# Kernel tuning notes

Hardware: AMD Instinct MI355X
Metric: run time of the kernel (lower is better)

The kernel has to match this reference:

```python
import jax, jax.numpy as jnp
import numpy as np

CODEBOOK_SIZE = 1024
EMBED_DIM = 64
COMMITMENT_COST = 0.25


def setup_inputs() -> dict:
    key = jax.random.key(0)
    k1, k2 = jax.random.split(key)
    z = jax.random.normal(k1, (8, EMBED_DIM, 8192), dtype=jnp.float32)
    # torch init: uniform(-1/codebook_size, 1/codebook_size)
    codebook_weight = jax.random.uniform(
        k2, (CODEBOOK_SIZE, EMBED_DIM), dtype=jnp.float32,
        minval=-1.0 / CODEBOOK_SIZE, maxval=1.0 / CODEBOOK_SIZE)
    return {"z": z, "codebook_weight": codebook_weight}


def reference(z, codebook_weight):
    B, D, T = z.shape
    # [B*T, D]
    z_flat = jnp.transpose(z, (0, 2, 1)).reshape(-1, D)
    # squared euclidean distances to each code: ||z||^2 - 2 z.W^T + ||W||^2
    distances = (jnp.sum(z_flat * z_flat, axis=1, keepdims=True)
                 - 2.0 * z_flat @ codebook_weight.T
                 + jnp.sum(codebook_weight * codebook_weight, axis=1))
    codes = jnp.argmin(distances, axis=1)  # [B*T]
    z_q = codebook_weight[codes].reshape(B, T, D).transpose(0, 2, 1)  # [B, D, T]
    commitment_loss = jnp.mean((jax.lax.stop_gradient(z_q) - z) ** 2)
    codebook_loss = jnp.mean((z_q - jax.lax.stop_gradient(z)) ** 2)
    vq_loss = codebook_loss + COMMITMENT_COST * commitment_loss
    # straight-through estimator
    z_q_st = z + jax.lax.stop_gradient(z_q - z)
    return z_q_st, vq_loss, codes
```

## Files before the change

### kernel.cpp

```cpp
#include <hip/hip_runtime.h>


#define T_DIM 8192
#define D_DIM 64
#define C_DIM 1024
#define B_DIM 8
#define NROWS (B_DIM * T_DIM)
#define NELEM (B_DIM * D_DIM * T_DIM)
#define NBLKS (NROWS / 256)

#define R64(M) M(0) M(1) M(2) M(3) M(4) M(5) M(6) M(7) \
  M(8) M(9) M(10) M(11) M(12) M(13) M(14) M(15) \
  M(16) M(17) M(18) M(19) M(20) M(21) M(22) M(23) \
  M(24) M(25) M(26) M(27) M(28) M(29) M(30) M(31) \
  M(32) M(33) M(34) M(35) M(36) M(37) M(38) M(39) \
  M(40) M(41) M(42) M(43) M(44) M(45) M(46) M(47) \
  M(48) M(49) M(50) M(51) M(52) M(53) M(54) M(55) \
  M(56) M(57) M(58) M(59) M(60) M(61) M(62) M(63)

#define SQ_(x) __fmul_rn(x, x)
#define AD_(a, b) __fadd_rn(a, b)

#define PAIRWISE64(p, dst) \
  float pr0 = SQ_(p##0);  pr0 = AD_(pr0, SQ_(p##8));  pr0 = AD_(pr0, SQ_(p##16)); pr0 = AD_(pr0, SQ_(p##24)); pr0 = AD_(pr0, SQ_(p##32)); pr0 = AD_(pr0, SQ_(p##40)); pr0 = AD_(pr0, SQ_(p##48)); pr0 = AD_(pr0, SQ_(p##56)); \
  float pr1 = SQ_(p##1);  pr1 = AD_(pr1, SQ_(p##9));  pr1 = AD_(pr1, SQ_(p##17)); pr1 = AD_(pr1, SQ_(p##25)); pr1 = AD_(pr1, SQ_(p##33)); pr1 = AD_(pr1, SQ_(p##41)); pr1 = AD_(pr1, SQ_(p##49)); pr1 = AD_(pr1, SQ_(p##57)); \
  float pr2 = SQ_(p##2);  pr2 = AD_(pr2, SQ_(p##10)); pr2 = AD_(pr2, SQ_(p##18)); pr2 = AD_(pr2, SQ_(p##26)); pr2 = AD_(pr2, SQ_(p##34)); pr2 = AD_(pr2, SQ_(p##42)); pr2 = AD_(pr2, SQ_(p##50)); pr2 = AD_(pr2, SQ_(p##58)); \
  float pr3 = SQ_(p##3);  pr3 = AD_(pr3, SQ_(p##11)); pr3 = AD_(pr3, SQ_(p##19)); pr3 = AD_(pr3, SQ_(p##27)); pr3 = AD_(pr3, SQ_(p##35)); pr3 = AD_(pr3, SQ_(p##43)); pr3 = AD_(pr3, SQ_(p##51)); pr3 = AD_(pr3, SQ_(p##59)); \
  float pr4 = SQ_(p##4);  pr4 = AD_(pr4, SQ_(p##12)); pr4 = AD_(pr4, SQ_(p##20)); pr4 = AD_(pr4, SQ_(p##28)); pr4 = AD_(pr4, SQ_(p##36)); pr4 = AD_(pr4, SQ_(p##44)); pr4 = AD_(pr4, SQ_(p##52)); pr4 = AD_(pr4, SQ_(p##60)); \
  float pr5 = SQ_(p##5);  pr5 = AD_(pr5, SQ_(p##13)); pr5 = AD_(pr5, SQ_(p##21)); pr5 = AD_(pr5, SQ_(p##29)); pr5 = AD_(pr5, SQ_(p##37)); pr5 = AD_(pr5, SQ_(p##45)); pr5 = AD_(pr5, SQ_(p##53)); pr5 = AD_(pr5, SQ_(p##61)); \
  float pr6 = SQ_(p##6);  pr6 = AD_(pr6, SQ_(p##14)); pr6 = AD_(pr6, SQ_(p##22)); pr6 = AD_(pr6, SQ_(p##30)); pr6 = AD_(pr6, SQ_(p##38)); pr6 = AD_(pr6, SQ_(p##46)); pr6 = AD_(pr6, SQ_(p##54)); pr6 = AD_(pr6, SQ_(p##62)); \
  float pr7 = SQ_(p##7);  pr7 = AD_(pr7, SQ_(p##15)); pr7 = AD_(pr7, SQ_(p##23)); pr7 = AD_(pr7, SQ_(p##31)); pr7 = AD_(pr7, SQ_(p##39)); pr7 = AD_(pr7, SQ_(p##47)); pr7 = AD_(pr7, SQ_(p##55)); pr7 = AD_(pr7, SQ_(p##63)); \
  float dst = AD_(AD_(AD_(pr0, pr1), AD_(pr2, pr3)), AD_(AD_(pr4, pr5), AD_(pr6, pr7)));

#define WSQ_OF(arr, dst) float dst; { \
  float c0 = SQ_(arr[0].x); c0=AD_(c0,SQ_(arr[2].x)); c0=AD_(c0,SQ_(arr[4].x)); c0=AD_(c0,SQ_(arr[6].x)); c0=AD_(c0,SQ_(arr[8].x)); c0=AD_(c0,SQ_(arr[10].x)); c0=AD_(c0,SQ_(arr[12].x)); c0=AD_(c0,SQ_(arr[14].x)); \
  float c1 = SQ_(arr[0].y); c1=AD_(c1,SQ_(arr[2].y)); c1=AD_(c1,SQ_(arr[4].y)); c1=AD_(c1,SQ_(arr[6].y)); c1=AD_(c1,SQ_(arr[8].y)); c1=AD_(c1,SQ_(arr[10].y)); c1=AD_(c1,SQ_(arr[12].y)); c1=AD_(c1,SQ_(arr[14].y)); \
  float c2 = SQ_(arr[0].z); c2=AD_(c2,SQ_(arr[2].z)); c2=AD_(c2,SQ_(arr[4].z)); c2=AD_(c2,SQ_(arr[6].z)); c2=AD_(c2,SQ_(arr[8].z)); c2=AD_(c2,SQ_(arr[10].z)); c2=AD_(c2,SQ_(arr[12].z)); c2=AD_(c2,SQ_(arr[14].z)); \
  float c3 = SQ_(arr[0].w); c3=AD_(c3,SQ_(arr[2].w)); c3=AD_(c3,SQ_(arr[4].w)); c3=AD_(c3,SQ_(arr[6].w)); c3=AD_(c3,SQ_(arr[8].w)); c3=AD_(c3,SQ_(arr[10].w)); c3=AD_(c3,SQ_(arr[12].w)); c3=AD_(c3,SQ_(arr[14].w)); \
  float c4 = SQ_(arr[1].x); c4=AD_(c4,SQ_(arr[3].x)); c4=AD_(c4,SQ_(arr[5].x)); c4=AD_(c4,SQ_(arr[7].x)); c4=AD_(c4,SQ_(arr[9].x)); c4=AD_(c4,SQ_(arr[11].x)); c4=AD_(c4,SQ_(arr[13].x)); c4=AD_(c4,SQ_(arr[15].x)); \
  float c5 = SQ_(arr[1].y); c5=AD_(c5,SQ_(arr[3].y)); c5=AD_(c5,SQ_(arr[5].y)); c5=AD_(c5,SQ_(arr[7].y)); c5=AD_(c5,SQ_(arr[9].y)); c5=AD_(c5,SQ_(arr[11].y)); c5=AD_(c5,SQ_(arr[13].y)); c5=AD_(c5,SQ_(arr[15].y)); \
  float c6 = SQ_(arr[1].z); c6=AD_(c6,SQ_(arr[3].z)); c6=AD_(c6,SQ_(arr[5].z)); c6=AD_(c6,SQ_(arr[7].z)); c6=AD_(c6,SQ_(arr[9].z)); c6=AD_(c6,SQ_(arr[11].z)); c6=AD_(c6,SQ_(arr[13].z)); c6=AD_(c6,SQ_(arr[15].z)); \
  float c7 = SQ_(arr[1].w); c7=AD_(c7,SQ_(arr[3].w)); c7=AD_(c7,SQ_(arr[5].w)); c7=AD_(c7,SQ_(arr[7].w)); c7=AD_(c7,SQ_(arr[9].w)); c7=AD_(c7,SQ_(arr[11].w)); c7=AD_(c7,SQ_(arr[13].w)); c7=AD_(c7,SQ_(arr[15].w)); \
  dst = AD_(AD_(AD_(c0, c1), AD_(c2, c3)), AD_(AD_(c4, c5), AD_(c6, c7))); }

__global__ __launch_bounds__(512, 2)
void vq_fused_kernel(const float* __restrict__ z,
                     const float* __restrict__ cb,
                     float* __restrict__ out,
                     float* __restrict__ codes,
                     double* __restrict__ partials) {
    const int tid  = threadIdx.x;
    const int wid  = tid >> 6;
    const int lane = tid & 63;
    const int row0 = blockIdx.x * 256;
    const int b    = row0 >> 13;
    const int t0   = row0 & (T_DIM - 1);

    __shared__ float4 zl[16][256];
    __shared__ float  zsql[256];
    __shared__ float2 res[8][256];
    __shared__ int    codesl[256];

    if (tid < 256) {
        const float* zp = z + (size_t)b * (D_DIM * T_DIM) + (t0 + tid);
#define LOADZ(k) float z##k = zp[(size_t)k * T_DIM];
        R64(LOADZ)
#undef LOADZ
        PAIRWISE64(z, zsq)
        zsql[tid] = zsq;
        zl[ 0][tid] = make_float4(z0,  z1,  z2,  z3);
        zl[ 1][tid] = make_float4(z4,  z5,  z6,  z7);
        zl[ 2][tid] = make_float4(z8,  z9,  z10, z11);
        zl[ 3][tid] = make_float4(z12, z13, z14, z15);
        zl[ 4][tid] = make_float4(z16, z17, z18, z19);
        zl[ 5][tid] = make_float4(z20, z21, z22, z23);
        zl[ 6][tid] = make_float4(z24, z25, z26, z27);
        zl[ 7][tid] = make_float4(z28, z29, z30, z31);
        zl[ 8][tid] = make_float4(z32, z33, z34, z35);
        zl[ 9][tid] = make_float4(z36, z37, z38, z39);
        zl[10][tid] = make_float4(z40, z41, z42, z43);
        zl[11][tid] = make_float4(z44, z45, z46, z47);
        zl[12][tid] = make_float4(z48, z49, z50, z51);
        zl[13][tid] = make_float4(z52, z53, z54, z55);
        zl[14][tid] = make_float4(z56, z57, z58, z59);
        zl[15][tid] = make_float4(z60, z61, z62, z63);
    }

    const int cbase = wid * 128;
    const int cA = cbase + lane;
    const int cB = cA + 64;
    float4 wa[16], wb[16];
    {
        const float4* wpa = (const float4*)(cb + ((size_t)cA << 6));
        const float4* wpb = (const float4*)(cb + ((size_t)cB << 6));
#pragma unroll
        for (int kk = 0; kk < 16; ++kk) { wa[kk] = wpa[kk]; wb[kk] = wpb[kk]; }
    }
    WSQ_OF(wa, wsqA)
    WSQ_OF(wb, wsqB)
    __syncthreads();

#pragma unroll 1
    for (int r = 0; r < 256; r += 4) {
        float aA0 = 0.f, aA1 = 0.f, aA2 = 0.f, aA3 = 0.f;
        float aB0 = 0.f, aB1 = 0.f, aB2 = 0.f, aB3 = 0.f;
#pragma unroll
        for (int kk = 0; kk < 16; ++kk) {
            const float4 zc0 = zl[kk][r + 0];
            const float4 zc1 = zl[kk][r + 1];
            const float4 zc2 = zl[kk][r + 2];
            const float4 zc3 = zl[kk][r + 3];
            const float4 WA = wa[kk];
            const float4 WB = wb[kk];
            aA0 = fmaf(zc0.x, WA.x, aA0); aA0 = fmaf(zc0.y, WA.y, aA0);
            aA0 = fmaf(zc0.z, WA.z, aA0); aA0 = fmaf(zc0.w, WA.w, aA0);
            aB0 = fmaf(zc0.x, WB.x, aB0); aB0 = fmaf(zc0.y, WB.y, aB0);
            aB0 = fmaf(zc0.z, WB.z, aB0); aB0 = fmaf(zc0.w, WB.w, aB0);
            aA1 = fmaf(zc1.x, WA.x, aA1); aA1 = fmaf(zc1.y, WA.y, aA1);
            aA1 = fmaf(zc1.z, WA.z, aA1); aA1 = fmaf(zc1.w, WA.w, aA1);
            aB1 = fmaf(zc1.x, WB.x, aB1); aB1 = fmaf(zc1.y, WB.y, aB1);
            aB1 = fmaf(zc1.z, WB.z, aB1); aB1 = fmaf(zc1.w, WB.w, aB1);
            aA2 = fmaf(zc2.x, WA.x, aA2); aA2 = fmaf(zc2.y, WA.y, aA2);
            aA2 = fmaf(zc2.z, WA.z, aA2); aA2 = fmaf(zc2.w, WA.w, aA2);
            aB2 = fmaf(zc2.x, WB.x, aB2); aB2 = fmaf(zc2.y, WB.y, aB2);
            aB2 = fmaf(zc2.z, WB.z, aB2); aB2 = fmaf(zc2.w, WB.w, aB2);
            aA3 = fmaf(zc3.x, WA.x, aA3); aA3 = fmaf(zc3.y, WA.y, aA3);
            aA3 = fmaf(zc3.z, WA.z, aA3); aA3 = fmaf(zc3.w, WA.w, aA3);
            aB3 = fmaf(zc3.x, WB.x, aB3); aB3 = fmaf(zc3.y, WB.y, aB3);
            aB3 = fmaf(zc3.z, WB.z, aB3); aB3 = fmaf(zc3.w, WB.w, aB3);
        }
        const float zr0 = zsql[r + 0];
        const float zr1 = zsql[r + 1];
        const float zr2 = zsql[r + 2];
        const float zr3 = zsql[r + 3];
        const float dA0 = __fadd_rn(__fsub_rn(zr0, __fmul_rn(2.0f, aA0)), wsqA);
        const float dB0 = __fadd_rn(__fsub_rn(zr0, __fmul_rn(2.0f, aB0)), wsqB);
        const float dA1 = __fadd_rn(__fsub_rn(zr1, __fmul_rn(2.0f, aA1)), wsqA);
        const float dB1 = __fadd_rn(__fsub_rn(zr1, __fmul_rn(2.0f, aB1)), wsqB);
        const float dA2 = __fadd_rn(__fsub_rn(zr2, __fmul_rn(2.0f, aA2)), wsqA);
        const float dB2 = __fadd_rn(__fsub_rn(zr2, __fmul_rn(2.0f, aB2)), wsqB);
        const float dA3 = __fadd_rn(__fsub_rn(zr3, __fmul_rn(2.0f, aA3)), wsqA);
        const float dB3 = __fadd_rn(__fsub_rn(zr3, __fmul_rn(2.0f, aB3)), wsqB);
        const bool tB0 = (dB0 < dA0); const float d0 = tB0 ? dB0 : dA0;
        const bool tB1 = (dB1 < dA1); const float d1 = tB1 ? dB1 : dA1;
        const bool tB2 = (dB2 < dA2); const float d2 = tB2 ? dB2 : dA2;
        const bool tB3 = (dB3 < dA3); const float d3 = tB3 ? dB3 : dA3;
        float m0 = d0, m1 = d1, m2 = d2, m3 = d3;
#pragma unroll
        for (int off = 32; off > 0; off >>= 1) {
            m0 = fminf(m0, __shfl_xor(m0, off, 64));
            m1 = fminf(m1, __shfl_xor(m1, off, 64));
            m2 = fminf(m2, __shfl_xor(m2, off, 64));
            m3 = fminf(m3, __shfl_xor(m3, off, 64));
        }
#define ARGMIN_J(mj, dj, tBj, outIdx) { \
        const unsigned long long mskA = __ballot((!tBj) && (dj == mj)); \
        const unsigned long long mskB = __ballot(tBj && (dj == mj)); \
        int code; \
        if (mskA) code = cbase + (__ffsll((long long)mskA) - 1); \
        else      code = cbase + 64 + (__ffsll((long long)mskB) - 1); \
        if (lane == 0) res[wid][outIdx] = make_float2(mj, (float)code); }
        ARGMIN_J(m0, d0, tB0, r + 0)
        ARGMIN_J(m1, d1, tB1, r + 1)
        ARGMIN_J(m2, d2, tB2, r + 2)
        ARGMIN_J(m3, d3, tB3, r + 3)
#undef ARGMIN_J
    }
    __syncthreads();

    if (tid < 256) {
        float2 best = res[0][tid];
#pragma unroll
        for (int w = 1; w < 8; ++w) {
            const float2 p = res[w][tid];
            if (p.x < best.x) best = p;
        }
        codes[row0 + tid] = best.y;
        codesl[tid] = (int)best.y;
    }
    __syncthreads();

    const int hi = tid >> 8;
    const int tl = tid & 255;
    double lsum = 0.0;
    float* outb = out + (size_t)b * (D_DIM * T_DIM);
#pragma unroll 1
    for (int it = 0; it < 32; ++it) {
        const int d = (it << 1) + hi;
        const int code = codesl[tl];
        const float4 zq4 = zl[d >> 2][tl];
        const float zv = (d & 3) == 0 ? zq4.x : (d & 3) == 1 ? zq4.y
                       : (d & 3) == 2 ? zq4.z : zq4.w;
        const float wv = cb[(code << 6) + d];
        const float df = __fsub_rn(wv, zv);
        outb[(size_t)d * T_DIM + (t0 + tl)] = __fadd_rn(zv, df);
        lsum += (double)df * (double)df;
    }
#pragma unroll
    for (int o2 = 32; o2 > 0; o2 >>= 1) lsum += __shfl_down(lsum, o2, 64);
    __shared__ double redd[8];
    if (lane == 0) redd[wid] = lsum;
    __syncthreads();
    if (tid == 0) {
        double t4 = ((redd[0] + redd[1]) + (redd[2] + redd[3]))
                  + ((redd[4] + redd[5]) + (redd[6] + redd[7]));
        partials[blockIdx.x] = t4;
    }
}

__global__ void vq_loss_kernel(const double* __restrict__ partials,
                               float* __restrict__ out_loss) {
    double s = 0.0;
    for (int i = threadIdx.x; i < NBLKS; i += 256) s += partials[i];
#pragma unroll
    for (int o = 32; o > 0; o >>= 1) s += __shfl_down(s, o, 64);
    __shared__ double red[4];
    if ((threadIdx.x & 63) == 0) red[threadIdx.x >> 6] = s;
    __syncthreads();
    if (threadIdx.x == 0) {
        double tot = (red[0] + red[1]) + (red[2] + red[3]);
        out_loss[0] = (float)(1.25 * tot / (double)NELEM);
    }
}

extern "C" void kernel_launch(void* const* d_in, const int* in_sizes, int n_in,
                              void* d_out, int out_size, void* d_ws, size_t ws_size,
                              hipStream_t stream) {
    const float* z  = (const float*)d_in[0];
    const float* cb = (const float*)d_in[1];

    float* out      = (float*)d_out;
    float* out_loss = out + NELEM;
    float* codes    = out + NELEM + 1;

    double* partials = (double*)d_ws;

    vq_fused_kernel<<<NBLKS, 512, 0, stream>>>(z, cb, out, codes, partials);
    vq_loss_kernel<<<1, 256, 0, stream>>>(partials, out_loss);
}
```

Before: 223.8 us.

## Halve block size and give each thread four codebook entries in registers

Each block now runs 256 threads instead of 512, and each wave covers 256 codes (four per lane, held in registers) instead of 128. This doubles the reuse of each shared-memory z read per FMA and halves the cross-wave argmin reduction. The epilogue is also rewritten so each thread handles one row and reads the codebook row as float4. In exchange, register pressure roughly doubles (64 float4 weights plus 16 accumulators) and occupancy drops to one block of 256 threads per launch bound, which risks spills or poor latency hiding.

```diff
diff --git a/kernel.cpp b/kernel.cpp
--- a/kernel.cpp
+++ b/kernel.cpp
@@ -43,7 +43,11 @@
   float c7 = SQ_(arr[1].w); c7=AD_(c7,SQ_(arr[3].w)); c7=AD_(c7,SQ_(arr[5].w)); c7=AD_(c7,SQ_(arr[7].w)); c7=AD_(c7,SQ_(arr[9].w)); c7=AD_(c7,SQ_(arr[11].w)); c7=AD_(c7,SQ_(arr[13].w)); c7=AD_(c7,SQ_(arr[15].w)); \
   dst = AD_(AD_(AD_(c0, c1), AD_(c2, c3)), AD_(AD_(c4, c5), AD_(c6, c7))); }
 
-__global__ __launch_bounds__(512, 2)
+#define FM4(acc, zc, W) \
+    acc = fmaf(zc.x, W.x, acc); acc = fmaf(zc.y, W.y, acc); \
+    acc = fmaf(zc.z, W.z, acc); acc = fmaf(zc.w, W.w, acc);
+
+__global__ __launch_bounds__(256, 1)
 void vq_fused_kernel(const float* __restrict__ z,
                      const float* __restrict__ cb,
                      float* __restrict__ out,
@@ -58,10 +62,10 @@
 
     __shared__ float4 zl[16][256];
     __shared__ float  zsql[256];
-    __shared__ float2 res[8][256];
+    __shared__ float2 res[4][256];
     __shared__ int    codesl[256];
 
-    if (tid < 256) {
+    {
         const float* zp = z + (size_t)b * (D_DIM * T_DIM) + (t0 + tid);
 #define LOADZ(k) float z##k = zp[(size_t)k * T_DIM];
         R64(LOADZ)
@@ -86,24 +90,31 @@
         zl[15][tid] = make_float4(z60, z61, z62, z63);
     }
 
-    const int cbase = wid * 128;
-    const int cA = cbase + lane;
-    const int cB = cA + 64;
-    float4 wa[16], wb[16];
+    const int cbase = wid * 256;
+    float4 wa[16], wb[16], wc[16], wd[16];
     {
-        const float4* wpa = (const float4*)(cb + ((size_t)cA << 6));
-        const float4* wpb = (const float4*)(cb + ((size_t)cB << 6));
-#pragma unroll
-        for (int kk = 0; kk < 16; ++kk) { wa[kk] = wpa[kk]; wb[kk] = wpb[kk]; }
+        const float4* wpa = (const float4*)(cb + ((size_t)(cbase + lane)       << 6));
+        const float4* wpb = (const float4*)(cb + ((size_t)(cbase + lane + 64)  << 6));
+        const float4* wpc = (const float4*)(cb + ((size_t)(cbase + lane + 128) << 6));
+        const float4* wpd = (const float4*)(cb + ((size_t)(cbase + lane + 192) << 6));
+#pragma unroll
+        for (int kk = 0; kk < 16; ++kk) {
+            wa[kk] = wpa[kk]; wb[kk] = wpb[kk];
+            wc[kk] = wpc[kk]; wd[kk] = wpd[kk];
+        }
     }
     WSQ_OF(wa, wsqA)
     WSQ_OF(wb, wsqB)
+    WSQ_OF(wc, wsqC)
+    WSQ_OF(wd, wsqD)
     __syncthreads();
 
 #pragma unroll 1
     for (int r = 0; r < 256; r += 4) {
         float aA0 = 0.f, aA1 = 0.f, aA2 = 0.f, aA3 = 0.f;
         float aB0 = 0.f, aB1 = 0.f, aB2 = 0.f, aB3 = 0.f;
+        float aC0 = 0.f, aC1 = 0.f, aC2 = 0.f, aC3 = 0.f;
+        float aD0 = 0.f, aD1 = 0.f, aD2 = 0.f, aD3 = 0.f;
 #pragma unroll
         for (int kk = 0; kk < 16; ++kk) {
             const float4 zc0 = zl[kk][r + 0];
@@ -112,22 +123,12 @@
             const float4 zc3 = zl[kk][r + 3];
             const float4 WA = wa[kk];
             const float4 WB = wb[kk];
-            aA0 = fmaf(zc0.x, WA.x, aA0); aA0 = fmaf(zc0.y, WA.y, aA0);
-            aA0 = fmaf(zc0.z, WA.z, aA0); aA0 = fmaf(zc0.w, WA.w, aA0);
-            aB0 = fmaf(zc0.x, WB.x, aB0); aB0 = fmaf(zc0.y, WB.y, aB0);
-            aB0 = fmaf(zc0.z, WB.z, aB0); aB0 = fmaf(zc0.w, WB.w, aB0);
-            aA1 = fmaf(zc1.x, WA.x, aA1); aA1 = fmaf(zc1.y, WA.y, aA1);
-            aA1 = fmaf(zc1.z, WA.z, aA1); aA1 = fmaf(zc1.w, WA.w, aA1);
-            aB1 = fmaf(zc1.x, WB.x, aB1); aB1 = fmaf(zc1.y, WB.y, aB1);
-            aB1 = fmaf(zc1.z, WB.z, aB1); aB1 = fmaf(zc1.w, WB.w, aB1);
-            aA2 = fmaf(zc2.x, WA.x, aA2); aA2 = fmaf(zc2.y, WA.y, aA2);
-            aA2 = fmaf(zc2.z, WA.z, aA2); aA2 = fmaf(zc2.w, WA.w, aA2);
-            aB2 = fmaf(zc2.x, WB.x, aB2); aB2 = fmaf(zc2.y, WB.y, aB2);
-            aB2 = fmaf(zc2.z, WB.z, aB2); aB2 = fmaf(zc2.w, WB.w, aB2);
-            aA3 = fmaf(zc3.x, WA.x, aA3); aA3 = fmaf(zc3.y, WA.y, aA3);
-            aA3 = fmaf(zc3.z, WA.z, aA3); aA3 = fmaf(zc3.w, WA.w, aA3);
-            aB3 = fmaf(zc3.x, WB.x, aB3); aB3 = fmaf(zc3.y, WB.y, aB3);
-            aB3 = fmaf(zc3.z, WB.z, aB3); aB3 = fmaf(zc3.w, WB.w, aB3);
+            const float4 WC = wc[kk];
+            const float4 WD = wd[kk];
+            FM4(aA0, zc0, WA) FM4(aA1, zc1, WA) FM4(aA2, zc2, WA) FM4(aA3, zc3, WA)
+            FM4(aB0, zc0, WB) FM4(aB1, zc1, WB) FM4(aB2, zc2, WB) FM4(aB3, zc3, WB)
+            FM4(aC0, zc0, WC) FM4(aC1, zc1, WC) FM4(aC2, zc2, WC) FM4(aC3, zc3, WC)
+            FM4(aD0, zc0, WD) FM4(aD1, zc1, WD) FM4(aD2, zc2, WD) FM4(aD3, zc3, WD)
         }
         const float zr0 = zsql[r + 0];
         const float zr1 = zsql[r + 1];
@@ -135,17 +136,24 @@
         const float zr3 = zsql[r + 3];
         const float dA0 = __fadd_rn(__fsub_rn(zr0, __fmul_rn(2.0f, aA0)), wsqA);
         const float dB0 = __fadd_rn(__fsub_rn(zr0, __fmul_rn(2.0f, aB0)), wsqB);
+        const float dC0 = __fadd_rn(__fsub_rn(zr0, __fmul_rn(2.0f, aC0)), wsqC);
+        const float dD0 = __fadd_rn(__fsub_rn(zr0, __fmul_rn(2.0f, aD0)), wsqD);
         const float dA1 = __fadd_rn(__fsub_rn(zr1, __fmul_rn(2.0f, aA1)), wsqA);
         const float dB1 = __fadd_rn(__fsub_rn(zr1, __fmul_rn(2.0f, aB1)), wsqB);
+        const float dC1 = __fadd_rn(__fsub_rn(zr1, __fmul_rn(2.0f, aC1)), wsqC);
+        const float dD1 = __fadd_rn(__fsub_rn(zr1, __fmul_rn(2.0f, aD1)), wsqD);
         const float dA2 = __fadd_rn(__fsub_rn(zr2, __fmul_rn(2.0f, aA2)), wsqA);
         const float dB2 = __fadd_rn(__fsub_rn(zr2, __fmul_rn(2.0f, aB2)), wsqB);
+        const float dC2 = __fadd_rn(__fsub_rn(zr2, __fmul_rn(2.0f, aC2)), wsqC);
+        const float dD2 = __fadd_rn(__fsub_rn(zr2, __fmul_rn(2.0f, aD2)), wsqD);
         const float dA3 = __fadd_rn(__fsub_rn(zr3, __fmul_rn(2.0f, aA3)), wsqA);
         const float dB3 = __fadd_rn(__fsub_rn(zr3, __fmul_rn(2.0f, aB3)), wsqB);
-        const bool tB0 = (dB0 < dA0); const float d0 = tB0 ? dB0 : dA0;
-        const bool tB1 = (dB1 < dA1); const float d1 = tB1 ? dB1 : dA1;
-        const bool tB2 = (dB2 < dA2); const float d2 = tB2 ? dB2 : dA2;
-        const bool tB3 = (dB3 < dA3); const float d3 = tB3 ? dB3 : dA3;
-        float m0 = d0, m1 = d1, m2 = d2, m3 = d3;
+        const float dC3 = __fadd_rn(__fsub_rn(zr3, __fmul_rn(2.0f, aC3)), wsqC);
+        const float dD3 = __fadd_rn(__fsub_rn(zr3, __fmul_rn(2.0f, aD3)), wsqD);
+        float m0 = fminf(fminf(dA0, dB0), fminf(dC0, dD0));
+        float m1 = fminf(fminf(dA1, dB1), fminf(dC1, dD1));
+        float m2 = fminf(fminf(dA2, dB2), fminf(dC2, dD2));
+        float m3 = fminf(fminf(dA3, dB3), fminf(dC3, dD3));
 #pragma unroll
         for (int off = 32; off > 0; off >>= 1) {
             m0 = fminf(m0, __shfl_xor(m0, off, 64));
@@ -153,25 +161,29 @@
             m2 = fminf(m2, __shfl_xor(m2, off, 64));
             m3 = fminf(m3, __shfl_xor(m3, off, 64));
         }
-#define ARGMIN_J(mj, dj, tBj, outIdx) { \
-        const unsigned long long mskA = __ballot((!tBj) && (dj == mj)); \
-        const unsigned long long mskB = __ballot(tBj && (dj == mj)); \
+#define ARG4(mj, dAj, dBj, dCj, dDj, outIdx) { \
+        const unsigned long long kA = __ballot(dAj == mj); \
+        const unsigned long long kB = __ballot(dBj == mj); \
+        const unsigned long long kC = __ballot(dCj == mj); \
+        const unsigned long long kD = __ballot(dDj == mj); \
         int code; \
-        if (mskA) code = cbase + (__ffsll((long long)mskA) - 1); \
-        else      code = cbase + 64 + (__ffsll((long long)mskB) - 1); \
+        if (kA)      code = cbase +       (__ffsll((long long)kA) - 1); \
+        else if (kB) code = cbase + 64  + (__ffsll((long long)kB) - 1); \
+        else if (kC) code = cbase + 128 + (__ffsll((long long)kC) - 1); \
+        else         code = cbase + 192 + (__ffsll((long long)kD) - 1); \
         if (lane == 0) res[wid][outIdx] = make_float2(mj, (float)code); }
-        ARGMIN_J(m0, d0, tB0, r + 0)
-        ARGMIN_J(m1, d1, tB1, r + 1)
-        ARGMIN_J(m2, d2, tB2, r + 2)
-        ARGMIN_J(m3, d3, tB3, r + 3)
-#undef ARGMIN_J
-    }
-    __syncthreads();
-
-    if (tid < 256) {
+        ARG4(m0, dA0, dB0, dC0, dD0, r + 0)
+        ARG4(m1, dA1, dB1, dC1, dD1, r + 1)
+        ARG4(m2, dA2, dB2, dC2, dD2, r + 2)
+        ARG4(m3, dA3, dB3, dC3, dD3, r + 3)
+#undef ARG4
+    }
+    __syncthreads();
+
+    {
         float2 best = res[0][tid];
 #pragma unroll
-        for (int w = 1; w < 8; ++w) {
+        for (int w = 1; w < 4; ++w) {
             const float2 p = res[w][tid];
             if (p.x < best.x) best = p;
         }
@@ -180,32 +192,32 @@
     }
     __syncthreads();
 
-    const int hi = tid >> 8;
-    const int tl = tid & 255;
+    const int tl = tid;
+    const int code = codesl[tl];
     double lsum = 0.0;
-    float* outb = out + (size_t)b * (D_DIM * T_DIM);
+    float* outb = out + (size_t)b * (D_DIM * T_DIM) + t0 + tl;
 #pragma unroll 1
-    for (int it = 0; it < 32; ++it) {
-        const int d = (it << 1) + hi;
-        const int code = codesl[tl];
-        const float4 zq4 = zl[d >> 2][tl];
-        const float zv = (d & 3) == 0 ? zq4.x : (d & 3) == 1 ? zq4.y
-                       : (d & 3) == 2 ? zq4.z : zq4.w;
-        const float wv = cb[(code << 6) + d];
-        const float df = __fsub_rn(wv, zv);
-        outb[(size_t)d * T_DIM + (t0 + tl)] = __fadd_rn(zv, df);
-        lsum += (double)df * (double)df;
+    for (int it = 0; it < 16; ++it) {
+        const float4 z4 = zl[it][tl];
+        const float4 w4 = *(const float4*)(cb + ((size_t)code << 6) + (it << 2));
+        const float df0 = __fsub_rn(w4.x, z4.x);
+        const float df1 = __fsub_rn(w4.y, z4.y);
+        const float df2 = __fsub_rn(w4.z, z4.z);
+        const float df3 = __fsub_rn(w4.w, z4.w);
+        outb[(size_t)((it << 2) + 0) * T_DIM] = __fadd_rn(z4.x, df0);
+        outb[(size_t)((it << 2) + 1) * T_DIM] = __fadd_rn(z4.y, df1);
+        outb[(size_t)((it << 2) + 2) * T_DIM] = __fadd_rn(z4.z, df2);
+        outb[(size_t)((it << 2) + 3) * T_DIM] = __fadd_rn(z4.w, df3);
+        lsum += (double)df0 * df0 + (double)df1 * df1
+              + (double)df2 * df2 + (double)df3 * df3;
     }
 #pragma unroll
     for (int o2 = 32; o2 > 0; o2 >>= 1) lsum += __shfl_down(lsum, o2, 64);
-    __shared__ double redd[8];
+    __shared__ double redd[4];
     if (lane == 0) redd[wid] = lsum;
     __syncthreads();
-    if (tid == 0) {
-        double t4 = ((redd[0] + redd[1]) + (redd[2] + redd[3]))
-                  + ((redd[4] + redd[5]) + (redd[6] + redd[7]));
-        partials[blockIdx.x] = t4;
-    }
+    if (tid == 0)
+        partials[blockIdx.x] = (redd[0] + redd[1]) + (redd[2] + redd[3]);
 }
 
 __global__ void vq_loss_kernel(const double* __restrict__ partials,
@@ -235,6 +247,6 @@
 
     double* partials = (double*)d_ws;
 
-    vq_fused_kernel<<<NBLKS, 512, 0, stream>>>(z, cb, out, codes, partials);
+    vq_fused_kernel<<<NBLKS, 256, 0, stream>>>(z, cb, out, codes, partials);
     vq_loss_kernel<<<1, 256, 0, stream>>>(partials, out_loss);
 }
```

After: 333.3 us. +48.9%, slower.

## Halve rows per block, load z with all threads, vectorize codebook gather

Applied to the files above, without the earlier changes.

Each block now handles 128 rows instead of 256, doubling the grid and halving shared memory per block, and the launch bounds ask for 4 blocks per CU. All 512 threads cooperatively load z into shared memory instead of only 256, and the output/loss epilogue gathers codebook rows as float4 with fixed per-thread slices. The intent is more occupancy and better latency hiding in the load and epilogue phases. In exchange, every block still loads all 128 codebook vectors per wave into registers, so codebook load and norm work per output row doubles, and the 4-block bound may cause register spills.

```diff
diff --git a/kernel.cpp b/kernel.cpp
--- a/kernel.cpp
+++ b/kernel.cpp
@@ -7,16 +7,8 @@
 #define B_DIM 8
 #define NROWS (B_DIM * T_DIM)
 #define NELEM (B_DIM * D_DIM * T_DIM)
-#define NBLKS (NROWS / 256)
-
-#define R64(M) M(0) M(1) M(2) M(3) M(4) M(5) M(6) M(7) \
-  M(8) M(9) M(10) M(11) M(12) M(13) M(14) M(15) \
-  M(16) M(17) M(18) M(19) M(20) M(21) M(22) M(23) \
-  M(24) M(25) M(26) M(27) M(28) M(29) M(30) M(31) \
-  M(32) M(33) M(34) M(35) M(36) M(37) M(38) M(39) \
-  M(40) M(41) M(42) M(43) M(44) M(45) M(46) M(47) \
-  M(48) M(49) M(50) M(51) M(52) M(53) M(54) M(55) \
-  M(56) M(57) M(58) M(59) M(60) M(61) M(62) M(63)
+#define TROWS 128
+#define NBLKS (NROWS / TROWS)
 
 #define SQ_(x) __fmul_rn(x, x)
 #define AD_(a, b) __fadd_rn(a, b)
@@ -43,7 +35,7 @@
   float c7 = SQ_(arr[1].w); c7=AD_(c7,SQ_(arr[3].w)); c7=AD_(c7,SQ_(arr[5].w)); c7=AD_(c7,SQ_(arr[7].w)); c7=AD_(c7,SQ_(arr[9].w)); c7=AD_(c7,SQ_(arr[11].w)); c7=AD_(c7,SQ_(arr[13].w)); c7=AD_(c7,SQ_(arr[15].w)); \
   dst = AD_(AD_(AD_(c0, c1), AD_(c2, c3)), AD_(AD_(c4, c5), AD_(c6, c7))); }
 
-__global__ __launch_bounds__(512, 2)
+__global__ __launch_bounds__(512, 4)
 void vq_fused_kernel(const float* __restrict__ z,
                      const float* __restrict__ cb,
                      float* __restrict__ out,
@@ -52,47 +44,62 @@
     const int tid  = threadIdx.x;
     const int wid  = tid >> 6;
     const int lane = tid & 63;
-    const int row0 = blockIdx.x * 256;
+    const int row0 = blockIdx.x * TROWS;
     const int b    = row0 >> 13;
     const int t0   = row0 & (T_DIM - 1);
 
-    __shared__ float4 zl[16][256];
-    __shared__ float  zsql[256];
-    __shared__ float2 res[8][256];
-    __shared__ int    codesl[256];
-
-    if (tid < 256) {
-        const float* zp = z + (size_t)b * (D_DIM * T_DIM) + (t0 + tid);
-#define LOADZ(k) float z##k = zp[(size_t)k * T_DIM];
-        R64(LOADZ)
-#undef LOADZ
+    __shared__ float4 zl[16][TROWS];
+    __shared__ float  zsql[TROWS];
+    __shared__ float2 res[8][TROWS];
+    __shared__ int    codesl[TROWS];
+
+    {
+        const int q   = tid >> 7;
+        const int row = tid & (TROWS - 1);
+        const float* zp = z + (size_t)b * (D_DIM * T_DIM)
+                        + (size_t)(q * 16) * T_DIM + (t0 + row);
+#pragma unroll
+        for (int j = 0; j < 4; ++j) {
+            float4 v;
+            v.x = zp[(size_t)(j * 4 + 0) * T_DIM];
+            v.y = zp[(size_t)(j * 4 + 1) * T_DIM];
+            v.z = zp[(size_t)(j * 4 + 2) * T_DIM];
+            v.w = zp[(size_t)(j * 4 + 3) * T_DIM];
+            zl[q * 4 + j][row] = v;
+        }
+    }
+    __syncthreads();
+
+    if (tid < TROWS) {
+        const float4 q0 = zl[0][tid],  q1 = zl[1][tid],  q2 = zl[2][tid],  q3 = zl[3][tid];
+        const float4 q4 = zl[4][tid],  q5 = zl[5][tid],  q6 = zl[6][tid],  q7 = zl[7][tid];
+        const float4 q8 = zl[8][tid],  q9 = zl[9][tid],  q10 = zl[10][tid], q11 = zl[11][tid];
+        const float4 q12 = zl[12][tid], q13 = zl[13][tid], q14 = zl[14][tid], q15 = zl[15][tid];
+        const float z0=q0.x,  z1=q0.y,  z2=q0.z,  z3=q0.w;
+        const float z4=q1.x,  z5=q1.y,  z6=q1.z,  z7=q1.w;
+        const float z8=q2.x,  z9=q2.y,  z10=q2.z, z11=q2.w;
+        const float z12=q3.x, z13=q3.y, z14=q3.z, z15=q3.w;
+        const float z16=q4.x, z17=q4.y, z18=q4.z, z19=q4.w;
+        const float z20=q5.x, z21=q5.y, z22=q5.z, z23=q5.w;
+        const float z24=q6.x, z25=q6.y, z26=q6.z, z27=q6.w;
+        const float z28=q7.x, z29=q7.y, z30=q7.z, z31=q7.w;
+        const float z32=q8.x, z33=q8.y, z34=q8.z, z35=q8.w;
+        const float z36=q9.x, z37=q9.y, z38=q9.z, z39=q9.w;
+        const float z40=q10.x, z41=q10.y, z42=q10.z, z43=q10.w;
+        const float z44=q11.x, z45=q11.y, z46=q11.z, z47=q11.w;
+        const float z48=q12.x, z49=q12.y, z50=q12.z, z51=q12.w;
+        const float z52=q13.x, z53=q13.y, z54=q13.z, z55=q13.w;
+        const float z56=q14.x, z57=q14.y, z58=q14.z, z59=q14.w;
+        const float z60=q15.x, z61=q15.y, z62=q15.z, z63=q15.w;
         PAIRWISE64(z, zsq)
         zsql[tid] = zsq;
-        zl[ 0][tid] = make_float4(z0,  z1,  z2,  z3);
-        zl[ 1][tid] = make_float4(z4,  z5,  z6,  z7);
-        zl[ 2][tid] = make_float4(z8,  z9,  z10, z11);
-        zl[ 3][tid] = make_float4(z12, z13, z14, z15);
-        zl[ 4][tid] = make_float4(z16, z17, z18, z19);
-        zl[ 5][tid] = make_float4(z20, z21, z22, z23);
-        zl[ 6][tid] = make_float4(z24, z25, z26, z27);
-        zl[ 7][tid] = make_float4(z28, z29, z30, z31);
-        zl[ 8][tid] = make_float4(z32, z33, z34, z35);
-        zl[ 9][tid] = make_float4(z36, z37, z38, z39);
-        zl[10][tid] = make_float4(z40, z41, z42, z43);
-        zl[11][tid] = make_float4(z44, z45, z46, z47);
-        zl[12][tid] = make_float4(z48, z49, z50, z51);
-        zl[13][tid] = make_float4(z52, z53, z54, z55);
-        zl[14][tid] = make_float4(z56, z57, z58, z59);
-        zl[15][tid] = make_float4(z60, z61, z62, z63);
     }
 
     const int cbase = wid * 128;
-    const int cA = cbase + lane;
-    const int cB = cA + 64;
     float4 wa[16], wb[16];
     {
-        const float4* wpa = (const float4*)(cb + ((size_t)cA << 6));
-        const float4* wpb = (const float4*)(cb + ((size_t)cB << 6));
+        const float4* wpa = (const float4*)(cb + ((size_t)(cbase + lane)      << 6));
+        const float4* wpb = (const float4*)(cb + ((size_t)(cbase + lane + 64) << 6));
 #pragma unroll
         for (int kk = 0; kk < 16; ++kk) { wa[kk] = wpa[kk]; wb[kk] = wpb[kk]; }
     }
@@ -101,7 +108,7 @@
     __syncthreads();
 
 #pragma unroll 1
-    for (int r = 0; r < 256; r += 4) {
+    for (int r = 0; r < TROWS; r += 4) {
         float aA0 = 0.f, aA1 = 0.f, aA2 = 0.f, aA3 = 0.f;
         float aB0 = 0.f, aB1 = 0.f, aB2 = 0.f, aB3 = 0.f;
 #pragma unroll
@@ -168,7 +175,7 @@
     }
     __syncthreads();
 
-    if (tid < 256) {
+    if (tid < TROWS) {
         float2 best = res[0][tid];
 #pragma unroll
         for (int w = 1; w < 8; ++w) {
@@ -180,21 +187,26 @@
     }
     __syncthreads();
 
-    const int hi = tid >> 8;
-    const int tl = tid & 255;
+    const int q   = tid >> 7;
+    const int row = tid & (TROWS - 1);
+    const int code = codesl[row];
     double lsum = 0.0;
-    float* outb = out + (size_t)b * (D_DIM * T_DIM);
-#pragma unroll 1
-    for (int it = 0; it < 32; ++it) {
-        const int d = (it << 1) + hi;
-        const int code = codesl[tl];
-        const float4 zq4 = zl[d >> 2][tl];
-        const float zv = (d & 3) == 0 ? zq4.x : (d & 3) == 1 ? zq4.y
-                       : (d & 3) == 2 ? zq4.z : zq4.w;
-        const float wv = cb[(code << 6) + d];
-        const float df = __fsub_rn(wv, zv);
-        outb[(size_t)d * T_DIM + (t0 + tl)] = __fadd_rn(zv, df);
-        lsum += (double)df * (double)df;
+    float* outb = out + (size_t)b * (D_DIM * T_DIM) + t0 + row;
+#pragma unroll
+    for (int j = 0; j < 4; ++j) {
+        const int it = q * 4 + j;
+        const float4 z4 = zl[it][row];
+        const float4 w4 = *(const float4*)(cb + ((size_t)code << 6) + (it << 2));
+        const float df0 = __fsub_rn(w4.x, z4.x);
+        const float df1 = __fsub_rn(w4.y, z4.y);
+        const float df2 = __fsub_rn(w4.z, z4.z);
+        const float df3 = __fsub_rn(w4.w, z4.w);
+        outb[(size_t)((it << 2) + 0) * T_DIM] = __fadd_rn(z4.x, df0);
+        outb[(size_t)((it << 2) + 1) * T_DIM] = __fadd_rn(z4.y, df1);
+        outb[(size_t)((it << 2) + 2) * T_DIM] = __fadd_rn(z4.z, df2);
+        outb[(size_t)((it << 2) + 3) * T_DIM] = __fadd_rn(z4.w, df3);
+        lsum += (double)df0 * df0 + (double)df1 * df1
+              + (double)df2 * df2 + (double)df3 * df3;
     }
 #pragma unroll
     for (int o2 = 32; o2 > 0; o2 >>= 1) lsum += __shfl_down(lsum, o2, 64);
@@ -202,9 +214,8 @@
     if (lane == 0) redd[wid] = lsum;
     __syncthreads();
     if (tid == 0) {
-        double t4 = ((redd[0] + redd[1]) + (redd[2] + redd[3]))
-                  + ((redd[4] + redd[5]) + (redd[6] + redd[7]));
-        partials[blockIdx.x] = t4;
+        partials[blockIdx.x] = ((redd[0] + redd[1]) + (redd[2] + redd[3]))
+                             + ((redd[4] + redd[5]) + (redd[6] + redd[7]));
     }
 }
 
```

Measured after the change: 302.7 us. 1.35x slower.
